# Kernel tuning notes

Measured on AMD Instinct MI355X. Metric: run time of the kernel, lower is better.

Reference implementation:

```python
import jax, jax.numpy as jnp
import numpy as np

N = 100000      # num_nodes
R = 8           # num_relations
D = 128         # hidden_dim
E = 600000      # num_edges
P = 100000      # num query pairs
PH = 128        # pair_hidden_dim


def _xavier(key, shape):
    fan_in, fan_out = shape[-2], shape[-1]
    limit = float(np.sqrt(6.0 / (fan_in + fan_out)))
    return jax.random.uniform(key, shape, jnp.float32, -limit, limit)


def setup_inputs() -> dict:
    key = jax.random.key(0)
    ks = jax.random.split(key, 16)
    edge_index = jax.random.randint(ks[0], (2, E), 0, N)
    edge_type = jax.random.randint(ks[1], (E,), 0, R)
    drug_index = jax.random.randint(ks[2], (P,), 0, N)
    disease_index = jax.random.randint(ks[3], (P,), 0, N)
    emb = _xavier(ks[4], (N, D))
    rw1 = _xavier(ks[5], (R, D, D))
    sl1 = _xavier(ks[6], (D, D))
    b1 = jnp.zeros((D,), jnp.float32)
    rw2 = _xavier(ks[7], (R, D, D))
    sl2 = _xavier(ks[8], (D, D))
    b2 = jnp.zeros((D,), jnp.float32)
    pw1 = _xavier(ks[9], (3 * D, PH))
    pb1 = jnp.zeros((PH,), jnp.float32)
    pw2 = _xavier(ks[10], (PH, 1))
    pb2 = jnp.zeros((1,), jnp.float32)
    return {
        "edge_index": edge_index, "edge_type": edge_type,
        "drug_index": drug_index, "disease_index": disease_index,
        "emb": emb, "rw1": rw1, "sl1": sl1, "b1": b1,
        "rw2": rw2, "sl2": sl2, "b2": b2,
        "pw1": pw1, "pb1": pb1, "pw2": pw2, "pb2": pb2,
    }


def _rgcn_layer(x, rel_w, self_w, bias, src, dst, etype):
    # Transform all node features once per relation: [R, N, D]
    xW = jnp.einsum('nd,rde->rne', x, rel_w)
    # Per-relation in-degree of dst (matches torch bincount-per-relation, clamp_min(1))
    seg_key = etype * N + dst                                  # [E]
    deg = jax.ops.segment_sum(jnp.ones((src.shape[0],), x.dtype), seg_key,
                              num_segments=R * N)
    deg = jnp.maximum(deg, 1.0)
    msg = xW[etype, src] / deg[seg_key][:, None]               # [E, D]
    agg = jax.ops.segment_sum(msg, dst, num_segments=N)        # [N, D]
    return x @ self_w + agg + bias


def reference(edge_index, edge_type, drug_index, disease_index,
              emb, rw1, sl1, b1, rw2, sl2, b2, pw1, pb1, pw2, pb2):
    src, dst = edge_index[0], edge_index[1]
    # encode (eval mode: dropout is identity)
    x = _rgcn_layer(emb, rw1, sl1, b1, src, dst, edge_type)
    x = jax.nn.relu(x)
    x = _rgcn_layer(x, rw2, sl2, b2, src, dst, edge_type)
    # score_pairs
    dh = x[drug_index]
    sh = x[disease_index]
    feat = jnp.concatenate((dh, sh, dh * sh), axis=-1)         # [P, 3D]
    h = jax.nn.relu(feat @ pw1 + pb1)
    logits = (h @ pw2 + pb2)[:, 0]                             # [P]
    return logits
```

## Files before the change

### kernel.cpp

```cpp
#include <hip/hip_runtime.h>

#define D 128
#define RMAX 16

typedef short s16x8 __attribute__((ext_vector_type(8)));
typedef float f32x4 __attribute__((ext_vector_type(4)));

__device__ inline unsigned short f2b(float f) {
    unsigned u = __builtin_bit_cast(unsigned, f);
    unsigned r = (u + 0x7FFFu + ((u >> 16) & 1u)) >> 16;
    return (unsigned short)r;
}
__device__ inline float b2f(unsigned short h) {
    unsigned u = ((unsigned)h) << 16;
    return __builtin_bit_cast(float, u);
}


__global__ void k_count2(const int* __restrict__ etype, const int* __restrict__ dstA,
                         int E, int N, int R,
                         int* __restrict__ deg, int* __restrict__ counts) {
    __shared__ int lh[RMAX];
    if (threadIdx.x < RMAX) lh[threadIdx.x] = 0;
    __syncthreads();
    int e = blockIdx.x * blockDim.x + threadIdx.x;
    if (e < E) {
        int r = etype[e];
        atomicAdd(&deg[r * N + dstA[e]], 1);
        atomicAdd(&lh[r], 1);
    }
    __syncthreads();
    if (threadIdx.x < R && lh[threadIdx.x])
        atomicAdd(&counts[threadIdx.x], lh[threadIdx.x]);
}

__global__ void k_offsets(const int* __restrict__ counts, int* __restrict__ po,
                          int R, int N) {
    if (threadIdx.x == 0 && blockIdx.x == 0) {
        int acc = 0;
        for (int r = 0; r < R; ++r) {
            po[r] = acc;
            acc += ((counts[r] + 127) / 128) * 128;
        }
        po[R] = acc;
        acc += ((N + 127) / 128) * 128;
        po[R + 1] = acc;
    }
}


template<int VPT>
__global__ void k_scan_blk(const int* __restrict__ in, int* __restrict__ tmp,
                           int* __restrict__ bsum, int n) {
    __shared__ int sd[256];
    int t = threadIdx.x;
    long base = (long)blockIdx.x * (256 * VPT) + (long)t * VPT;
    int s[VPT];
    int tsum = 0;
    #pragma unroll
    for (int k = 0; k < VPT; ++k) { s[k] = (base + k < n) ? in[base + k] : 0; tsum += s[k]; }
    sd[t] = tsum;
    __syncthreads();
    for (int off = 1; off < 256; off <<= 1) {
        int v = (t >= off) ? sd[t - off] : 0;
        __syncthreads();
        sd[t] += v;
        __syncthreads();
    }
    int run = sd[t] - tsum;
    #pragma unroll
    for (int k = 0; k < VPT; ++k) { if (base + k < n) tmp[base + k] = run; run += s[k]; }
    if (t == 255) bsum[blockIdx.x] = sd[255];
}

__global__ void k_scan2(const int* __restrict__ bsum, int* __restrict__ boff, int nb) {
    __shared__ int sd[256];
    int t = threadIdx.x;
    int v = (t < nb) ? bsum[t] : 0;
    sd[t] = v;
    __syncthreads();
    for (int off = 1; off < 256; off <<= 1) {
        int w = (t >= off) ? sd[t - off] : 0;
        __syncthreads();
        sd[t] += w;
        __syncthreads();
    }
    if (t < nb) boff[t] = sd[t] - v;
}

__global__ void k_scan3(const int* __restrict__ tmp, const int* __restrict__ boff,
                        int* __restrict__ out, int n, int shift) {
    int i = blockIdx.x * 256 + threadIdx.x;
    if (i < n) out[i] = tmp[i] + boff[i >> shift];
}


__global__ void k_scatter3(const int* __restrict__ etype, const int* __restrict__ srcA,
                           const int* __restrict__ dstA, int E, int N, int R,
                           const int* __restrict__ degOff, const int* __restrict__ po,
                           int* __restrict__ binCur, int* __restrict__ slotSrc) {
    int t = blockIdx.x * 256 + threadIdx.x;
    if (t < E) {
        int r = etype[t];
        int bin = r * N + dstA[t];
        int rank = atomicAdd(&binCur[bin], 1);
        int pos = po[r] + (degOff[bin] - degOff[r * N]) + rank;
        slotSrc[pos] = srcA[t];
    } else if (t < E + N) {
        int n = t - E;
        slotSrc[po[R] + n] = n;
    }
}


__global__ void k_prep(const float* __restrict__ emb,
                       const float* __restrict__ rw1, const float* __restrict__ sl1,
                       const float* __restrict__ rw2, const float* __restrict__ sl2,
                       const float* __restrict__ pw1,
                       unsigned short* __restrict__ embb,
                       unsigned short* __restrict__ wAll1,
                       unsigned short* __restrict__ wAll2,
                       unsigned short* __restrict__ pw1T,
                       int N, int R)
{
    long t = (long)blockIdx.x * 256 + threadIdx.x;
    long u0 = (long)N * D / 4;
    if (t < u0) {
        long i = t * 4;
        f32x4 v = *(const f32x4*)(emb + i);
        unsigned a0 = (unsigned)f2b(v[0]) | ((unsigned)f2b(v[1]) << 16);
        unsigned a1 = (unsigned)f2b(v[2]) | ((unsigned)f2b(v[3]) << 16);
        uint2 o; o.x = a0; o.y = a1;
        *(uint2*)(embb + i) = o;
        return;
    }
    t -= u0;
    long uW = (long)(R + 1) * D * D;
    if (t < 2 * uW) {
        const float* rw = (t < uW) ? rw1 : rw2;
        const float* sl = (t < uW) ? sl1 : sl2;
        unsigned short* o = (t < uW) ? wAll1 : wAll2;
        long u = (t < uW) ? t : t - uW;
        int r = (int)(u >> 14);
        int nb = (int)(u & 16383);
        int n = nb >> 7, kk = nb & 127;
        float v = (r < R) ? rw[((size_t)r * D + kk) * D + n] : sl[(size_t)kk * D + n];
        o[u] = f2b(v);
        return;
    }
    t -= 2 * uW;
    if (t < 3 * D * D) {
        int n = (int)(t / 384), ck = (int)(t - n * 384);
        int ch = ck >> 7, kl = (ck & 127) ^ ((n & 7) << 3);
        pw1T[t] = f2b(pw1[(size_t)(ch * 128 + kl) * 128 + n]);
    }
}


__global__ __launch_bounds__(256, 4) void k_gemm_msg(
    const unsigned short* __restrict__ xb,
    const unsigned short* __restrict__ wAll,
    const int* __restrict__ slotSrc,
    const int* __restrict__ po, int R,
    unsigned short* __restrict__ y)
{
    __shared__ unsigned char stg[32768];
    int tid = threadIdx.x;
    int row0 = blockIdx.x * 128;
    if (row0 >= po[R + 1]) return;
    int r = 0;
    while (row0 >= po[r + 1]) ++r;

    int lane = tid & 63, wid = tid >> 6;
    int lo = lane & 15, hi = lane >> 4;

    int r0g = wid * 32 + lo, r1g = r0g + 16;
    int sv0 = slotSrc[row0 + r0g];
    int sv1 = slotSrc[row0 + r1g];
    const unsigned short* xrow0 = xb + (size_t)sv0 * D;
    const unsigned short* xrow1 = xb + (size_t)sv1 * D;
    s16x8 a0[4], a1[4];
    #pragma unroll
    for (int ks = 0; ks < 4; ++ks) {
        a0[ks] = *(const s16x8*)(xrow0 + ks * 32 + hi * 8);
        a1[ks] = *(const s16x8*)(xrow1 + ks * 32 + hi * 8);
    }

    f32x4 acc[2][8];
    #pragma unroll
    for (int q = 0; q < 2; ++q)
        #pragma unroll
        for (int n = 0; n < 8; ++n) acc[q][n] = (f32x4){0, 0, 0, 0};

    const unsigned short* Bp = wAll + (size_t)r * D * D;
    #pragma unroll
    for (int ks = 0; ks < 4; ++ks) {
        #pragma unroll
        for (int n = 0; n < 8; ++n) {
            s16x8 bf = *(const s16x8*)(Bp + (size_t)(n * 16 + lo) * D + ks * 32 + hi * 8);
            acc[0][n] = __builtin_amdgcn_mfma_f32_16x16x32_bf16(a0[ks], bf, acc[0][n], 0, 0, 0);
            acc[1][n] = __builtin_amdgcn_mfma_f32_16x16x32_bf16(a1[ks], bf, acc[1][n], 0, 0, 0);
        }
    }

    unsigned char* wreg = stg + wid * 8192;
    #pragma unroll
    for (int m2 = 0; m2 < 2; ++m2) {
        #pragma unroll
        for (int reg = 0; reg < 4; ++reg) {
            int rloc = m2 * 16 + hi * 4 + reg;
            #pragma unroll
            for (int n = 0; n < 8; ++n) {
                int byteoff = rloc * 256 + (((n * 32 + (lo >> 3) * 16) ^ ((rloc & 7) << 4)) + (lo & 7) * 2);
                *(unsigned short*)(wreg + byteoff) = f2b(acc[m2][n][reg]);
            }
        }
    }
    {
        int m = lane >> 1, half = lane & 1;
        unsigned short* dst = y + (size_t)(row0 + wid * 32 + m) * D;
        #pragma unroll
        for (int i = 0; i < 8; ++i) {
            int c = half * 8 + i;
            int4 v = *(const int4*)(wreg + m * 256 + ((c * 16) ^ ((m & 7) << 4)));
            *(int4*)(dst + c * 8) = v;
        }
    }
}


template<bool RELU>
__global__ void k_reduce2(const unsigned short* __restrict__ y,
                          const int* __restrict__ degOff,
                          const int* __restrict__ po,
                          const float* __restrict__ bias,
                          unsigned short* __restrict__ out, int N, int R, int E)
{
    __shared__ int rbase[RMAX + 1];
    int tid = threadIdx.x;
    if (tid <= R) rbase[tid] = (tid < R) ? (po[tid] - degOff[(size_t)tid * N]) : po[R];
    __syncthreads();

    int team = tid >> 4, cj = tid & 15;
    float b[8];
    *(f32x4*)(b)     = *(const f32x4*)(bias + cj * 8);
    *(f32x4*)(b + 4) = *(const f32x4*)(bias + cj * 8 + 4);
    int dbase = blockIdx.x * 64 + team * 4;
    for (int i = 0; i < 4; ++i) {
        int d = dbase + i;
        if (d >= N) return;
        float a[8];
        {
            int4 v = *(const int4*)(y + (size_t)(rbase[R] + d) * D + cj * 8);
            const unsigned short* hp = (const unsigned short*)&v;
            #pragma unroll
            for (int j = 0; j < 8; ++j) a[j] = b[j] + b2f(hp[j]);
        }
        for (int r = 0; r < R; ++r) {
            int bin = r * N + d;
            int o0 = degOff[bin];
            int o1 = (bin + 1 < R * N) ? degOff[bin + 1] : E;
            int len = o1 - o0;
            if (!len) continue;
            long start = rbase[r] + o0;
            float s8[8];
            #pragma unroll
            for (int j = 0; j < 8; ++j) s8[j] = 0.0f;
            for (int q = 0; q < len; ++q) {
                int4 v = *(const int4*)(y + (size_t)(start + q) * D + cj * 8);
                const unsigned short* hp = (const unsigned short*)&v;
                #pragma unroll
                for (int j = 0; j < 8; ++j) s8[j] += b2f(hp[j]);
            }
            float inv = 1.0f / (float)len;
            #pragma unroll
            for (int j = 0; j < 8; ++j) a[j] = fmaf(s8[j], inv, a[j]);
        }
        unsigned short o[8];
        #pragma unroll
        for (int j = 0; j < 8; ++j) {
            float v = RELU ? fmaxf(a[j], 0.0f) : a[j];
            o[j] = f2b(v);
        }
        *(int4*)(out + (size_t)d * D + cj * 8) = *(const int4*)o;
    }
}


__global__ __launch_bounds__(256) void k_score(
    const unsigned short* __restrict__ x2b,
    const int* __restrict__ drug, const int* __restrict__ dis,
    const unsigned short* __restrict__ pw1T,
    const float* __restrict__ pb1, const float* __restrict__ pw2,
    const float* __restrict__ pb2, float* __restrict__ outp, int P)
{
    __shared__ unsigned char smA[32768];
    __shared__ unsigned char smB[32768];
    __shared__ float pb1s[128];
    __shared__ float pw2s[128];
    int tid = threadIdx.x;
    long p0 = (long)blockIdx.x * 128;
    if (tid < 128) { pb1s[tid] = pb1[tid]; pw2s[tid] = pw2[tid]; }
    float pb2v = pb2[0];

    int lane = tid & 63, wid = tid >> 6;
    int lo = lane & 15, hi = lane >> 4;
    f32x4 acc[2][8];
    #pragma unroll
    for (int q = 0; q < 2; ++q)
        #pragma unroll
        for (int b = 0; b < 8; ++b) acc[q][b] = (f32x4){0, 0, 0, 0};

    for (int chn = 0; chn < 3; ++chn) {
        {
            const int4* src = (const int4*)pw1T;
            int4* dstl = (int4*)smB;
            #pragma unroll
            for (int i = 0; i < 8; ++i) {
                int q = tid + i * 256;
                int n = q >> 4, c = q & 15;
                dstl[q] = src[n * 48 + chn * 16 + c];
            }
        }
        {
            int m = tid >> 1, half = tid & 1;
            long p = p0 + m;
            int4 z = {0, 0, 0, 0};
            if (p < P) {
                const int4* da = (const int4*)(x2b + (size_t)drug[p] * D);
                const int4* db = (const int4*)(x2b + (size_t)dis[p] * D);
                for (int c = half * 8; c < half * 8 + 8; ++c) {
                    int4 v;
                    if (chn == 0) v = da[c];
                    else if (chn == 1) v = db[c];
                    else {
                        int4 va = da[c], vb = db[c];
                        const unsigned short* ap = (const unsigned short*)&va;
                        const unsigned short* bp = (const unsigned short*)&vb;
                        unsigned short o[8];
                        #pragma unroll
                        for (int j = 0; j < 8; ++j) o[j] = f2b(b2f(ap[j]) * b2f(bp[j]));
                        v = *(const int4*)o;
                    }
                    *(int4*)(smA + m * 256 + ((c * 16) ^ ((m & 7) << 4))) = v;
                }
            } else {
                for (int c = half * 8; c < half * 8 + 8; ++c)
                    *(int4*)(smA + m * 256 + ((c * 16) ^ ((m & 7) << 4))) = z;
            }
        }
        __syncthreads();

        #pragma unroll
        for (int ks = 0; ks < 4; ++ks) {
            int kb = ks * 64 + hi * 16;
            int r0 = wid * 32 + lo, r1 = r0 + 16;
            s16x8 a0 = *(const s16x8*)(smA + r0 * 256 + (kb ^ ((r0 & 7) << 4)));
            s16x8 a1 = *(const s16x8*)(smA + r1 * 256 + (kb ^ ((r1 & 7) << 4)));
            #pragma unroll
            for (int n = 0; n < 8; ++n) {
                int cr = n * 16 + lo;
                s16x8 bf = *(const s16x8*)(smB + cr * 256 + (kb ^ ((cr & 7) << 4)));
                acc[0][n] = __builtin_amdgcn_mfma_f32_16x16x32_bf16(a0, bf, acc[0][n], 0, 0, 0);
                acc[1][n] = __builtin_amdgcn_mfma_f32_16x16x32_bf16(a1, bf, acc[1][n], 0, 0, 0);
            }
        }
        __syncthreads();
    }

    #pragma unroll
    for (int m2 = 0; m2 < 2; ++m2)
        #pragma unroll
        for (int reg = 0; reg < 4; ++reg) {
            float s = 0.0f;
            #pragma unroll
            for (int n = 0; n < 8; ++n) {
                int col = n * 16 + lo;
                float v = acc[m2][n][reg] + pb1s[col];
                v = fmaxf(v, 0.0f);
                s = fmaf(v, pw2s[col], s);
            }
            s += __shfl_xor(s, 1, 64);
            s += __shfl_xor(s, 2, 64);
            s += __shfl_xor(s, 4, 64);
            s += __shfl_xor(s, 8, 64);
            long p = p0 + wid * 32 + m2 * 16 + hi * 4 + reg;
            if (lo == 0 && p < P) outp[p] = s + pb2v;
        }
}


extern "C" void kernel_launch(void* const* d_in, const int* in_sizes, int n_in,
                              void* d_out, int out_size, void* d_ws, size_t ws_size,
                              hipStream_t stream) {
    const int*   edge_index = (const int*)d_in[0];
    const int*   edge_type  = (const int*)d_in[1];
    const int*   drug       = (const int*)d_in[2];
    const int*   dis        = (const int*)d_in[3];
    const float* emb        = (const float*)d_in[4];
    const float* rw1        = (const float*)d_in[5];
    const float* sl1        = (const float*)d_in[6];
    const float* b1         = (const float*)d_in[7];
    const float* rw2        = (const float*)d_in[8];
    const float* sl2        = (const float*)d_in[9];
    const float* b2         = (const float*)d_in[10];
    const float* pw1        = (const float*)d_in[11];
    const float* pb1        = (const float*)d_in[12];
    const float* pw2        = (const float*)d_in[13];
    const float* pb2        = (const float*)d_in[14];

    const int E = in_sizes[1];
    const int P = in_sizes[2];
    const int N = in_sizes[4] / D;
    const int R = in_sizes[5] / (D * D);

    const int* srcA = edge_index;
    const int* dstA = edge_index + E;

    const int slotN = E + N + 128 * (R + 2);

    char* ws = (char*)d_ws;
    unsigned short* embb = (unsigned short*)ws; ws += (size_t)N * D * 2;
    unsigned short* x1b  = (unsigned short*)ws; ws += (size_t)N * D * 2;
    unsigned short* y    = (unsigned short*)ws; ws += (size_t)slotN * D * 2;
    unsigned short* wAll1 = (unsigned short*)ws; ws += (size_t)(R + 1) * D * D * 2;
    unsigned short* wAll2 = (unsigned short*)ws; ws += (size_t)(R + 1) * D * D * 2;
    unsigned short* pw1T  = (unsigned short*)ws; ws += (size_t)3 * D * D * 2;
    int*   deg     = (int*)ws;   ws += (size_t)R * N * 4;
    int*   binCur  = (int*)ws;   ws += (size_t)R * N * 4;
    int*   counts  = (int*)ws;   ws += 256;
    int*   slotSrc = (int*)ws;   ws += (size_t)slotN * 4;
    size_t zbytes = (size_t)(2 * R * N + 64 + slotN) * 4;
    int* degOff  = (int*)ws; ws += (size_t)R * N * 4;
    int* bsum    = (int*)ws; ws += 256 * 4;
    int* boff    = (int*)ws; ws += 256 * 4;
    int* po      = (int*)ws; ws += 256;
    unsigned short* x2b = embb;

    hipMemsetAsync(deg, 0, zbytes, stream);

    long u0 = (long)N * D / 4;
    long uW = (long)(R + 1) * D * D;
    long utot = u0 + 2 * uW + 3 * D * D;
    k_prep<<<(int)((utot + 255) / 256), 256, 0, stream>>>(emb, rw1, sl1, rw2, sl2, pw1,
                                                          embb, wAll1, wAll2, pw1T, N, R);

    k_count2<<<(E + 255) / 256, 256, 0, stream>>>(edge_type, dstA, E, N, R, deg, counts);
    k_offsets<<<1, 1, 0, stream>>>(counts, po, R, N);

    int nbS = (R * N + 4095) / 4096;
    k_scan_blk<16><<<nbS, 256, 0, stream>>>(deg, degOff, bsum, R * N);
    k_scan2<<<1, 256, 0, stream>>>(bsum, boff, nbS);
    k_scan3<<<(R * N + 255) / 256, 256, 0, stream>>>(degOff, boff, degOff, R * N, 12);

    k_scatter3<<<(E + N + 255) / 256, 256, 0, stream>>>(edge_type, srcA, dstA, E, N, R,
                                                        degOff, po, binCur, slotSrc);

    int gridM = (E + 127) / 128 + (N + 127) / 128 + R + 2;
    int gridR = (N + 63) / 64;

    k_gemm_msg<<<gridM, 256, 0, stream>>>(embb, wAll1, slotSrc, po, R, y);
    k_reduce2<true><<<gridR, 256, 0, stream>>>(y, degOff, po, b1, x1b, N, R, E);
    k_gemm_msg<<<gridM, 256, 0, stream>>>(x1b, wAll2, slotSrc, po, R, y);
    k_reduce2<false><<<gridR, 256, 0, stream>>>(y, degOff, po, b2, x2b, N, R, E);
    k_score<<<(P + 127) / 128, 256, 0, stream>>>(x2b, drug, dis, pw1T, pb1, pw2, pb2,
                                                 (float*)d_out, P);
}
```

Baseline: 561.1 us.

## Stage swizzled relation weights in LDS for gather GEMM and halve shared buffer

The weight prep now stores each relation's bf16 weight matrix with an XOR swizzle on the k index. The message GEMM stages that matrix into LDS in two 64-column halves with cooperative int4 loads, replacing per-wave direct global loads of B fragments. The output staging reuses the same 16KB buffer in two halves, and the launch-bounds occupancy hint is dropped. This is meant to cut redundant global/L2 traffic for B and reduce LDS footprint, at the cost of extra block-wide barriers.

```diff
diff --git a/kernel.cpp b/kernel.cpp
--- a/kernel.cpp
+++ b/kernel.cpp
@@ -144,7 +144,8 @@
         int r = (int)(u >> 14);
         int nb = (int)(u & 16383);
         int n = nb >> 7, kk = nb & 127;
-        float v = (r < R) ? rw[((size_t)r * D + kk) * D + n] : sl[(size_t)kk * D + n];
+        int ke = kk ^ ((n & 7) << 3);
+        float v = (r < R) ? rw[((size_t)r * D + ke) * D + n] : sl[(size_t)ke * D + n];
         o[u] = f2b(v);
         return;
     }
@@ -157,14 +158,14 @@
 }
 
 
-__global__ __launch_bounds__(256, 4) void k_gemm_msg(
+__global__ __launch_bounds__(256) void k_gemm_msg(
     const unsigned short* __restrict__ xb,
     const unsigned short* __restrict__ wAll,
     const int* __restrict__ slotSrc,
     const int* __restrict__ po, int R,
     unsigned short* __restrict__ y)
 {
-    __shared__ unsigned char stg[32768];
+    __shared__ unsigned char smB[16384];
     int tid = threadIdx.x;
     int row0 = blockIdx.x * 128;
     if (row0 >= po[R + 1]) return;
@@ -192,38 +193,56 @@
         #pragma unroll
         for (int n = 0; n < 8; ++n) acc[q][n] = (f32x4){0, 0, 0, 0};
 
-    const unsigned short* Bp = wAll + (size_t)r * D * D;
-    #pragma unroll
-    for (int ks = 0; ks < 4; ++ks) {
-        #pragma unroll
-        for (int n = 0; n < 8; ++n) {
-            s16x8 bf = *(const s16x8*)(Bp + (size_t)(n * 16 + lo) * D + ks * 32 + hi * 8);
-            acc[0][n] = __builtin_amdgcn_mfma_f32_16x16x32_bf16(a0[ks], bf, acc[0][n], 0, 0, 0);
-            acc[1][n] = __builtin_amdgcn_mfma_f32_16x16x32_bf16(a1[ks], bf, acc[1][n], 0, 0, 0);
-        }
-    }
-
-    unsigned char* wreg = stg + wid * 8192;
-    #pragma unroll
-    for (int m2 = 0; m2 < 2; ++m2) {
-        #pragma unroll
-        for (int reg = 0; reg < 4; ++reg) {
-            int rloc = m2 * 16 + hi * 4 + reg;
-            #pragma unroll
-            for (int n = 0; n < 8; ++n) {
-                int byteoff = rloc * 256 + (((n * 32 + (lo >> 3) * 16) ^ ((rloc & 7) << 4)) + (lo & 7) * 2);
-                *(unsigned short*)(wreg + byteoff) = f2b(acc[m2][n][reg]);
-            }
-        }
-    }
-    {
-        int m = lane >> 1, half = lane & 1;
-        unsigned short* dst = y + (size_t)(row0 + wid * 32 + m) * D;
-        #pragma unroll
-        for (int i = 0; i < 8; ++i) {
-            int c = half * 8 + i;
-            int4 v = *(const int4*)(wreg + m * 256 + ((c * 16) ^ ((m & 7) << 4)));
-            *(int4*)(dst + c * 8) = v;
+    const int4* wsrc = (const int4*)(wAll + (size_t)r * D * D);
+
+    #pragma unroll
+    for (int h = 0; h < 2; ++h) {
+        if (h) __syncthreads();
+        {
+            int4* dstl = (int4*)smB;
+            #pragma unroll
+            for (int i = 0; i < 4; ++i)
+                dstl[tid + i * 256] = wsrc[h * 1024 + tid + i * 256];
+        }
+        __syncthreads();
+        #pragma unroll
+        for (int ks = 0; ks < 4; ++ks) {
+            int kb = ks * 64 + hi * 16;
+            #pragma unroll
+            for (int n2 = 0; n2 < 4; ++n2) {
+                int cloc = n2 * 16 + lo;
+                s16x8 bf = *(const s16x8*)(smB + cloc * 256 + (kb ^ ((cloc & 7) << 4)));
+                acc[0][h * 4 + n2] = __builtin_amdgcn_mfma_f32_16x16x32_bf16(a0[ks], bf, acc[0][h * 4 + n2], 0, 0, 0);
+                acc[1][h * 4 + n2] = __builtin_amdgcn_mfma_f32_16x16x32_bf16(a1[ks], bf, acc[1][h * 4 + n2], 0, 0, 0);
+            }
+        }
+    }
+
+    #pragma unroll
+    for (int h = 0; h < 2; ++h) {
+        __syncthreads();
+        #pragma unroll
+        for (int g = 0; g < 2; ++g) {
+            #pragma unroll
+            for (int reg = 0; reg < 4; ++reg) {
+                int rl = wid * 32 + g * 16 + hi * 4 + reg;
+                #pragma unroll
+                for (int n2 = 0; n2 < 4; ++n2) {
+                    int byteoff = rl * 128 + (((n2 * 32 + (lo >> 3) * 16) ^ ((rl & 7) << 4)) + (lo & 7) * 2);
+                    *(unsigned short*)(smB + byteoff) = f2b(acc[g][h * 4 + n2][reg]);
+                }
+            }
+        }
+        __syncthreads();
+        {
+            int m = tid >> 1, half2 = tid & 1;
+            unsigned short* dst = y + (size_t)(row0 + m) * D + h * 64 + half2 * 32;
+            #pragma unroll
+            for (int i = 0; i < 4; ++i) {
+                int c = half2 * 4 + i;
+                int4 v = *(const int4*)(smB + m * 128 + ((c * 16) ^ ((m & 7) << 4)));
+                *(int4*)(dst + i * 8) = v;
+            }
         }
     }
 }
```

After: 471.1 us. 1.19x faster.
